# Performance work log

Measured on AMD Instinct MI355X. Metric: run time of the kernel, lower is better.

## Reference

```python
import jax, jax.numpy as jnp
import numpy as np

B, C, CI, T, H, W = 2, 1024, 512, 32, 14, 14
N = T * H * W


def setup_inputs() -> dict:
    key = jax.random.key(0)
    ks = jax.random.split(key, 6)
    s_in = 1.0 / np.sqrt(C)
    s_mid = 1.0 / np.sqrt(CI)
    return {
        "x": jax.random.normal(ks[0], (B, C, T, H, W), jnp.float32),
        "Wk": jax.random.normal(ks[1], (CI, C), jnp.float32) * s_in,
        "bk": jnp.zeros((CI,), jnp.float32),
        "Wq": jax.random.normal(ks[2], (CI, C), jnp.float32) * s_in,
        "bq": jnp.zeros((CI,), jnp.float32),
        "Wv": jax.random.normal(ks[3], (CI, C), jnp.float32) * s_in,
        "bv": jnp.zeros((CI,), jnp.float32),
        "Wo": jax.random.normal(ks[4], (C, CI), jnp.float32) * s_mid,
        "bo": jnp.zeros((C,), jnp.float32),
    }


def reference(x, Wk, bk, Wq, bq, Wv, bv, Wo, bo):
    # x: (B, C, T, H, W). Dropout layers are identity at inference.
    b, c, t, h, w = x.shape
    n = t * h * w
    xf = x.reshape(b, c, n)                          # (B, C, N)
    k = jnp.einsum("dc,bcn->bdn", Wk, xf) + bk[None, :, None]   # (B, CI, N)
    q = jnp.einsum("dc,bcn->bdn", Wq, xf) + bq[None, :, None]   # (B, CI, N)
    v = jnp.einsum("dc,bcn->bdn", Wv, xf) + bv[None, :, None]   # (B, CI, N)
    # alpha[b,i,j] = sum_d key[b,i,d] * query[b,d,j], scaled by 1/T
    alpha = jnp.einsum("bdi,bdj->bij", k, q) / float(t)          # (B, N, N)
    alpha = jax.nn.softmax(alpha, axis=-1)
    # y (B, CI, N) with y[b,c,i] = sum_j alpha[b,i,j] * v[b,c,j]
    y = jnp.einsum("bij,bcj->bci", alpha, v)
    out = jnp.einsum("dc,bcn->bdn", Wo, y) + bo[None, :, None]   # (B, C, N)
    return out.reshape(b, c, t, h, w) + x
```

## Files before the change

kernel.cpp:

```cpp
#include <hip/hip_runtime.h>

#define Bb 2
#define Cc 1024
#define CIi 512
#define Nn 6272
#define JH 3136
#define SCALE (1.0f / 32.0f)

typedef __bf16 bf16;
typedef __bf16 bf16x8 __attribute__((ext_vector_type(8)));
typedef float f32x4 __attribute__((ext_vector_type(4)));
typedef unsigned int u32;
typedef unsigned char u8;
typedef unsigned int u32x4 __attribute__((ext_vector_type(4)));

__device__ __forceinline__ void g2l16(const void* g, void* l) {
  __builtin_amdgcn_global_load_lds(
      (const __attribute__((address_space(1))) u32*)g,
      (__attribute__((address_space(3))) u32*)(size_t)l, 16, 0, 0);
}

__device__ __forceinline__ u8 to_fp8(float v) {
  return (u8)(__builtin_amdgcn_cvt_pk_fp8_f32(v, v, 0, 0) & 0xff);
}

__global__ __launch_bounds__(256) void xpose_kernel(const float* __restrict__ x,
                                                    bf16* __restrict__ xT) {
  __shared__ float tile[32][33];
  int b = blockIdx.z;
  int n0 = blockIdx.x * 32, c0 = blockIdx.y * 32;
  int tn = threadIdx.x & 31, tr = threadIdx.x >> 5;
  const float* xp = x + ((size_t)b * Cc + c0) * Nn + n0;
  for (int i = 0; i < 4; i++) {
    int c = tr + i * 8;
    tile[c][tn] = xp[(size_t)c * Nn + tn];
  }
  __syncthreads();
  bf16* op = xT + ((size_t)b * Nn + n0) * Cc + c0;
  for (int i = 0; i < 4; i++) {
    int n = tr + i * 8;
    op[(size_t)n * Cc + tn] = (bf16)tile[tn][n];
  }
}

__global__ __launch_bounds__(256) void proj_kernel(
    const bf16* __restrict__ xT, const float* __restrict__ Wk,
    const float* __restrict__ Wq, const float* __restrict__ Wv,
    const float* __restrict__ bk, const float* __restrict__ bq,
    const float* __restrict__ bv, u8* __restrict__ kT8, u8* __restrict__ qT8,
    bf16* __restrict__ vv) {
  int z = blockIdx.z;
  int b = z / 3, proj = z % 3;
  const float* W = proj == 0 ? Wk : (proj == 1 ? Wq : Wv);
  const float* bias = proj == 0 ? bk : (proj == 1 ? bq : bv);
  int m0 = blockIdx.x * 128;
  int d0 = blockIdx.y * 128;
  __shared__ __align__(16) bf16 la[128 * 40];
  __shared__ __align__(16) bf16 lb[128 * 40];
  int tid = threadIdx.x;
  int wave = tid >> 6, lane = tid & 63, quad = lane >> 4, l16 = lane & 15;
  int wm = (wave >> 1) * 64, wn = (wave & 1) * 64;
  int row2 = tid >> 1, half = tid & 1;

  f32x4 acc[4][4] = {};
  const bf16* aSrc = xT + ((size_t)b * Nn + m0) * Cc;
  const float* bSrc = W + (size_t)(d0 + row2) * Cc;

  for (int k0 = 0; k0 < Cc; k0 += 32) {
    const u32x4* ga = (const u32x4*)(aSrc + (size_t)row2 * Cc + k0 + half * 16);
    u32x4 a0 = ga[0], a1 = ga[1];
    const f32x4* gb = (const f32x4*)(bSrc + k0 + half * 16);
    f32x4 w0 = gb[0], w1 = gb[1], w2 = gb[2], w3 = gb[3];
    *(u32x4*)&la[row2 * 40 + half * 16] = a0;
    *(u32x4*)&la[row2 * 40 + half * 16 + 8] = a1;
    bf16x8 p0 = {(bf16)w0[0], (bf16)w0[1], (bf16)w0[2], (bf16)w0[3],
                 (bf16)w1[0], (bf16)w1[1], (bf16)w1[2], (bf16)w1[3]};
    bf16x8 p1 = {(bf16)w2[0], (bf16)w2[1], (bf16)w2[2], (bf16)w2[3],
                 (bf16)w3[0], (bf16)w3[1], (bf16)w3[2], (bf16)w3[3]};
    *(bf16x8*)&lb[row2 * 40 + half * 16] = p0;
    *(bf16x8*)&lb[row2 * 40 + half * 16 + 8] = p1;
    __syncthreads();
    bf16x8 af[4], bfr[4];
    for (int t = 0; t < 4; t++)
      af[t] = *(const bf16x8*)&la[(wm + t * 16 + l16) * 40 + quad * 8];
    for (int t = 0; t < 4; t++)
      bfr[t] = *(const bf16x8*)&lb[(wn + t * 16 + l16) * 40 + quad * 8];
    for (int tm = 0; tm < 4; tm++)
      for (int tn = 0; tn < 4; tn++)
        acc[tm][tn] = __builtin_amdgcn_mfma_f32_16x16x32_bf16(
            af[tm], bfr[tn], acc[tm][tn], 0, 0, 0);
    __syncthreads();
  }
  for (int tn = 0; tn < 4; tn++) {
    int dcol = d0 + wn + tn * 16 + l16;
    float bval = bias[dcol];
    for (int tm = 0; tm < 4; tm++) {
      int nbase = m0 + wm + tm * 16 + quad * 4;
      for (int r = 0; r < 4; r++) {
        float val = acc[tm][tn][r] + bval;
        int nrow = nbase + r;
        if (proj == 0) {
          kT8[((size_t)b * Nn + nrow) * CIi + dcol] = to_fp8(val);
        } else if (proj == 1) {
          int ch = (dcol >> 3) ^ (nrow & 15);
          qT8[((size_t)b * Nn + nrow) * CIi + ch * 8 + (dcol & 7)] =
              to_fp8(val);
        } else {
          vv[((size_t)b * CIi + dcol) * Nn + nrow] = (bf16)val;
        }
      }
    }
  }
}

__global__ __launch_bounds__(512, 2) void attn_kernel(
    const u8* __restrict__ kT8, const u8* __restrict__ qT8,
    const bf16* __restrict__ vv, bf16* __restrict__ yp,
    float* __restrict__ ml) {
  int l = blockIdx.x;
  int jh = l & 1, b = (l >> 1) & 1;
  int i0 = (l >> 2) * 128;
  int tid = threadIdx.x;
  int wave = tid >> 6, lane = tid & 63, quad = lane >> 4, l16 = lane & 15;
  int wi = wave & 3, wj = wave >> 2;
  int dw = wave * 64;

  __shared__ __align__(16) u8 lq[2][64 * 512];
  __shared__ __align__(16) bf16 Psm[128 * 72];
  __shared__ float redw[2][128];
  __shared__ float redi[128];

  const u8* qb = qT8 + ((size_t)b * Nn + (size_t)jh * JH) * CIi;
  const bf16* vb = vv + (size_t)b * CIi * Nn + (size_t)jh * JH;

  long kf[2][16];
  {
    const u8* kp =
        kT8 + ((size_t)b * Nn + i0 + wi * 32 + l16) * CIi + quad * 8;
#pragma unroll
    for (int h = 0; h < 2; h++)
#pragma unroll
      for (int kk = 0; kk < 16; kk++)
        kf[h][kk] = *(const long*)(kp + (size_t)(h * 16) * CIi + kk * 32);
  }
  f32x4 oacc[8][4] = {};
  f32x4 l_acc[2] = {};

  {
    const u8* qrow = qb + (size_t)(wave * 8) * CIi + lane * 16;
#pragma unroll
    for (int r = 0; r < 4; r++)
      g2l16(qrow + r * 1024, &lq[0][(wave * 8) * 512 + r * 1024]);
  }
  __syncthreads();

  for (int j0 = 0; j0 < JH; j0 += 64) {
    int t = (j0 >> 6) & 1;
    u32x4 vf0[4];
#pragma unroll
    for (int ds = 0; ds < 4; ds++)
      vf0[ds] = *(const u32x4*)(vb + (size_t)(dw + ds * 16 + l16) * Nn + j0 +
                                quad * 8);
    __builtin_amdgcn_sched_barrier(0);
    if (j0 + 64 < JH) {
      const u8* qrow = qb + (size_t)(j0 + 64 + wave * 8) * CIi + lane * 16;
#pragma unroll
      for (int r = 0; r < 4; r++)
        g2l16(qrow + r * 1024, &lq[t ^ 1][(wave * 8) * 512 + r * 1024]);
    }
    f32x4 s00 = {}, s01 = {}, s10 = {}, s11 = {};
    {
      const u8* q0 = &lq[t][(wj * 32 + l16) * 512];
      const u8* q1 = &lq[t][(wj * 32 + 16 + l16) * 512];
#pragma unroll
      for (int kk = 0; kk < 16; kk++) {
        int sl = ((kk * 4 + quad) ^ l16) * 8;
        long qf0 = *(const long*)(q0 + sl);
        long qf1 = *(const long*)(q1 + sl);
        s00 = __builtin_amdgcn_mfma_f32_16x16x32_fp8_fp8(kf[0][kk], qf0, s00,
                                                         0, 0, 0);
        s01 = __builtin_amdgcn_mfma_f32_16x16x32_fp8_fp8(kf[0][kk], qf1, s01,
                                                         0, 0, 0);
        s10 = __builtin_amdgcn_mfma_f32_16x16x32_fp8_fp8(kf[1][kk], qf0, s10,
                                                         0, 0, 0);
        s11 = __builtin_amdgcn_mfma_f32_16x16x32_fp8_fp8(kf[1][kk], qf1, s11,
                                                         0, 0, 0);
      }
    }
    {
#pragma unroll
      for (int h = 0; h < 2; h++)
#pragma unroll
        for (int jb = 0; jb < 2; jb++) {
          const f32x4& sv = h == 0 ? (jb == 0 ? s00 : s01)
                                   : (jb == 0 ? s10 : s11);
#pragma unroll
          for (int r = 0; r < 4; r++) {
            float p = __expf(fminf(fmaf(sv[r], SCALE, -2.0f), 20.0f));
            l_acc[h][r] += p;
            int gi = wi * 32 + h * 16 + quad * 4 + r;
            int gj = wj * 32 + jb * 16 + l16;
            Psm[gi * 72 + gj] = (bf16)p;
          }
        }
    }
    asm volatile("s_waitcnt lgkmcnt(0)" ::: "memory");
    __builtin_amdgcn_s_barrier();
    asm volatile("" ::: "memory");

    {
#pragma unroll
      for (int is = 0; is < 8; is++) {
        bf16x8 pf = *(const bf16x8*)&Psm[(is * 16 + l16) * 72 + quad * 8];
#pragma unroll
        for (int ds = 0; ds < 4; ds++)
          oacc[is][ds] = __builtin_amdgcn_mfma_f32_16x16x32_bf16(
              pf, __builtin_bit_cast(bf16x8, vf0[ds]), oacc[is][ds], 0, 0, 0);
      }
      u32x4 vf1[4];
#pragma unroll
      for (int ds = 0; ds < 4; ds++)
        vf1[ds] = *(const u32x4*)(vb + (size_t)(dw + ds * 16 + l16) * Nn + j0 +
                                  32 + quad * 8);
#pragma unroll
      for (int is = 0; is < 8; is++) {
        bf16x8 pf =
            *(const bf16x8*)&Psm[(is * 16 + l16) * 72 + 32 + quad * 8];
#pragma unroll
        for (int ds = 0; ds < 4; ds++)
          oacc[is][ds] = __builtin_amdgcn_mfma_f32_16x16x32_bf16(
              pf, __builtin_bit_cast(bf16x8, vf1[ds]), oacc[is][ds], 0, 0, 0);
      }
    }
    __syncthreads();
  }

#pragma unroll
  for (int o = 1; o < 16; o <<= 1)
#pragma unroll
    for (int h = 0; h < 2; h++)
#pragma unroll
      for (int r = 0; r < 4; r++) l_acc[h][r] += __shfl_xor(l_acc[h][r], o);
  if (l16 == 0) {
#pragma unroll
    for (int h = 0; h < 2; h++)
#pragma unroll
      for (int r = 0; r < 4; r++)
        redw[wj][wi * 32 + h * 16 + quad * 4 + r] = l_acc[h][r];
  }
  __syncthreads();
  if (tid < 128) {
    float s = redw[0][tid] + redw[1][tid];
    ml[(size_t)(jh * Bb + b) * Nn + i0 + tid] = s;
    redi[tid] = 1.0f / s;
  }
  __syncthreads();
  bf16* ypb = yp + ((size_t)jh * Bb + b) * Nn * CIi;
#pragma unroll
  for (int is = 0; is < 8; is++) {
    f32x4 inv = *(const f32x4*)&redi[is * 16 + quad * 4];
#pragma unroll
    for (int ds = 0; ds < 4; ds++)
#pragma unroll
      for (int r = 0; r < 4; r++)
        ypb[(size_t)(i0 + is * 16 + quad * 4 + r) * CIi + dw + ds * 16 + l16] =
            (bf16)(oacc[is][ds][r] * inv[r]);
  }
}

__global__ __launch_bounds__(256) void merge_kernel(const bf16* __restrict__ yp,
                                                    const float* __restrict__ ml,
                                                    bf16* __restrict__ y) {
  int idx = blockIdx.x * 256 + threadIdx.x;
  int row = idx >> 6, c = idx & 63;
  float l0 = ml[row];
  float l1 = ml[(size_t)Bb * Nn + row];
  float inv = 1.0f / (l0 + l1);
  float w0 = l0 * inv, w1 = l1 * inv;
  bf16x8 v0 = *(const bf16x8*)&yp[(size_t)row * CIi + c * 8];
  bf16x8 v1 =
      *(const bf16x8*)&yp[(size_t)Bb * Nn * CIi + (size_t)row * CIi + c * 8];
  bf16x8 o;
#pragma unroll
  for (int k = 0; k < 8; k++)
    o[k] = (bf16)(w0 * (float)v0[k] + w1 * (float)v1[k]);
  *(bf16x8*)&y[(size_t)row * CIi + c * 8] = o;
}

__global__ __launch_bounds__(256) void out_kernel(
    const bf16* __restrict__ y, const float* __restrict__ Wo,
    const float* __restrict__ bo, const float* __restrict__ x,
    float* __restrict__ out) {
  int b = blockIdx.z;
  int d0 = blockIdx.x * 128;
  int m0 = blockIdx.y * 128;
  __shared__ __align__(16) bf16 la[128 * 40];
  __shared__ __align__(16) bf16 lb[128 * 40];
  int tid = threadIdx.x;
  int wave = tid >> 6, lane = tid & 63, quad = lane >> 4, l16 = lane & 15;
  int wm = (wave >> 1) * 64, wn = (wave & 1) * 64;
  int row2 = tid >> 1, half = tid & 1;
  f32x4 acc[4][4] = {};
  const float* aSrc = Wo + (size_t)(d0 + row2) * CIi;
  const bf16* bSrc = y + ((size_t)b * Nn + m0 + row2) * CIi;
  for (int k0 = 0; k0 < CIi; k0 += 32) {
    const f32x4* ga = (const f32x4*)(aSrc + k0 + half * 16);
    f32x4 w0 = ga[0], w1 = ga[1], w2 = ga[2], w3 = ga[3];
    const u32x4* gb = (const u32x4*)(bSrc + k0 + half * 16);
    u32x4 b0 = gb[0], b1 = gb[1];
    bf16x8 p0 = {(bf16)w0[0], (bf16)w0[1], (bf16)w0[2], (bf16)w0[3],
                 (bf16)w1[0], (bf16)w1[1], (bf16)w1[2], (bf16)w1[3]};
    bf16x8 p1 = {(bf16)w2[0], (bf16)w2[1], (bf16)w2[2], (bf16)w2[3],
                 (bf16)w3[0], (bf16)w3[1], (bf16)w3[2], (bf16)w3[3]};
    *(bf16x8*)&la[row2 * 40 + half * 16] = p0;
    *(bf16x8*)&la[row2 * 40 + half * 16 + 8] = p1;
    *(u32x4*)&lb[row2 * 40 + half * 16] = b0;
    *(u32x4*)&lb[row2 * 40 + half * 16 + 8] = b1;
    __syncthreads();
    bf16x8 af[4], bfr[4];
    for (int t = 0; t < 4; t++)
      af[t] = *(const bf16x8*)&la[(wm + t * 16 + l16) * 40 + quad * 8];
    for (int t = 0; t < 4; t++)
      bfr[t] = *(const bf16x8*)&lb[(wn + t * 16 + l16) * 40 + quad * 8];
    for (int tm = 0; tm < 4; tm++)
      for (int tn = 0; tn < 4; tn++)
        acc[tm][tn] = __builtin_amdgcn_mfma_f32_16x16x32_bf16(
            af[tm], bfr[tn], acc[tm][tn], 0, 0, 0);
    __syncthreads();
  }
  for (int tm = 0; tm < 4; tm++) {
    for (int r = 0; r < 4; r++) {
      int drow = d0 + wm + tm * 16 + quad * 4 + r;
      float bval = bo[drow];
      const float* xrow = x + ((size_t)b * Cc + drow) * Nn;
      float* orow = out + ((size_t)b * Cc + drow) * Nn;
      for (int tn = 0; tn < 4; tn++) {
        int ncol = m0 + wn + tn * 16 + l16;
        orow[ncol] = acc[tm][tn][r] + bval + xrow[ncol];
      }
    }
  }
}

extern "C" void kernel_launch(void* const* d_in, const int* in_sizes, int n_in,
                              void* d_out, int out_size, void* d_ws,
                              size_t ws_size, hipStream_t stream) {
  (void)in_sizes;
  (void)n_in;
  (void)out_size;
  (void)ws_size;
  const float* x = (const float*)d_in[0];
  const float* Wk = (const float*)d_in[1];
  const float* bk = (const float*)d_in[2];
  const float* Wq = (const float*)d_in[3];
  const float* bq = (const float*)d_in[4];
  const float* Wv = (const float*)d_in[5];
  const float* bv = (const float*)d_in[6];
  const float* Wo = (const float*)d_in[7];
  const float* bo = (const float*)d_in[8];
  float* out = (float*)d_out;

  bf16* xT = (bf16*)d_ws;
  bf16* yp = (bf16*)d_ws;
  bf16* y = (bf16*)d_ws + (size_t)Bb * Nn * Cc;
  u8* kT8 = (u8*)d_out;
  u8* qT8 = kT8 + (size_t)Bb * Nn * CIi;
  bf16* vv = (bf16*)(qT8 + (size_t)Bb * Nn * CIi);
  float* ml = (float*)((char*)d_out + (size_t)40 * 1024 * 1024);

  xpose_kernel<<<dim3(Nn / 32, Cc / 32, Bb), 256, 0, stream>>>(x, xT);
  proj_kernel<<<dim3(Nn / 128, CIi / 128, 3 * Bb), 256, 0, stream>>>(
      xT, Wk, Wq, Wv, bk, bq, bv, kT8, qT8, vv);
  attn_kernel<<<dim3((Nn / 128) * 2 * Bb), 512, 0, stream>>>(kT8, qT8, vv, yp,
                                                             ml);
  merge_kernel<<<dim3(Bb * Nn * 64 / 256), 256, 0, stream>>>(yp, ml, y);
  out_kernel<<<dim3(Cc / 128, Nn / 128, Bb), 256, 0, stream>>>(y, Wo, bo, x,
                                                               out);
}
```

Baseline: 598.7 us.

## Give each wave full 16-row by 64-column score strip, drop cross-wave row-sum reduction

Changes the QK^T work split so each of the 8 waves owns 16 query-key rows across all 64 columns instead of a 32x32 sub-block, halving K fragment registers and removing the cross-wave redw reduction and one barrier at the end. Both V fragment halves are now loaded up front at the start of each iteration instead of loading the second half mid-PV. This trades fewer K registers for more LDS Q reads per wave (4 Q rows per kk instead of 2) and more live V registers.

```diff
diff --git a/kernel.cpp b/kernel.cpp
--- a/kernel.cpp
+++ b/kernel.cpp
@@ -122,29 +122,25 @@
   int i0 = (l >> 2) * 128;
   int tid = threadIdx.x;
   int wave = tid >> 6, lane = tid & 63, quad = lane >> 4, l16 = lane & 15;
-  int wi = wave & 3, wj = wave >> 2;
   int dw = wave * 64;
 
   __shared__ __align__(16) u8 lq[2][64 * 512];
   __shared__ __align__(16) bf16 Psm[128 * 72];
-  __shared__ float redw[2][128];
   __shared__ float redi[128];
 
   const u8* qb = qT8 + ((size_t)b * Nn + (size_t)jh * JH) * CIi;
   const bf16* vb = vv + (size_t)b * CIi * Nn + (size_t)jh * JH;
 
-  long kf[2][16];
+  long kf[16];
   {
-    const u8* kp =
-        kT8 + ((size_t)b * Nn + i0 + wi * 32 + l16) * CIi + quad * 8;
-#pragma unroll
-    for (int h = 0; h < 2; h++)
-#pragma unroll
-      for (int kk = 0; kk < 16; kk++)
-        kf[h][kk] = *(const long*)(kp + (size_t)(h * 16) * CIi + kk * 32);
+    const u8* kp = kT8 + ((size_t)b * Nn + i0 + wave * 16 + l16) * CIi +
+                   quad * 8;
+#pragma unroll
+    for (int kk = 0; kk < 16; kk++)
+      kf[kk] = *(const long*)(kp + kk * 32);
   }
   f32x4 oacc[8][4] = {};
-  f32x4 l_acc[2] = {};
+  f32x4 l_acc = {};
 
   {
     const u8* qrow = qb + (size_t)(wave * 8) * CIi + lane * 16;
@@ -156,11 +152,13 @@
 
   for (int j0 = 0; j0 < JH; j0 += 64) {
     int t = (j0 >> 6) & 1;
-    u32x4 vf0[4];
-#pragma unroll
-    for (int ds = 0; ds < 4; ds++)
-      vf0[ds] = *(const u32x4*)(vb + (size_t)(dw + ds * 16 + l16) * Nn + j0 +
-                                quad * 8);
+    u32x4 vf[2][4];
+#pragma unroll
+    for (int jc = 0; jc < 2; jc++)
+#pragma unroll
+      for (int ds = 0; ds < 4; ds++)
+        vf[jc][ds] = *(const u32x4*)(vb + (size_t)(dw + ds * 16 + l16) * Nn +
+                                     j0 + jc * 32 + quad * 8);
     __builtin_amdgcn_sched_barrier(0);
     if (j0 + 64 < JH) {
       const u8* qrow = qb + (size_t)(j0 + 64 + wave * 8) * CIi + lane * 16;
@@ -168,91 +166,68 @@
       for (int r = 0; r < 4; r++)
         g2l16(qrow + r * 1024, &lq[t ^ 1][(wave * 8) * 512 + r * 1024]);
     }
-    f32x4 s00 = {}, s01 = {}, s10 = {}, s11 = {};
+    f32x4 s[4] = {};
     {
-      const u8* q0 = &lq[t][(wj * 32 + l16) * 512];
-      const u8* q1 = &lq[t][(wj * 32 + 16 + l16) * 512];
+      const u8* q0 = &lq[t][l16 * 512];
 #pragma unroll
       for (int kk = 0; kk < 16; kk++) {
         int sl = ((kk * 4 + quad) ^ l16) * 8;
         long qf0 = *(const long*)(q0 + sl);
-        long qf1 = *(const long*)(q1 + sl);
-        s00 = __builtin_amdgcn_mfma_f32_16x16x32_fp8_fp8(kf[0][kk], qf0, s00,
-                                                         0, 0, 0);
-        s01 = __builtin_amdgcn_mfma_f32_16x16x32_fp8_fp8(kf[0][kk], qf1, s01,
-                                                         0, 0, 0);
-        s10 = __builtin_amdgcn_mfma_f32_16x16x32_fp8_fp8(kf[1][kk], qf0, s10,
-                                                         0, 0, 0);
-        s11 = __builtin_amdgcn_mfma_f32_16x16x32_fp8_fp8(kf[1][kk], qf1, s11,
-                                                         0, 0, 0);
+        long qf1 = *(const long*)(q0 + 16 * 512 + sl);
+        long qf2 = *(const long*)(q0 + 32 * 512 + sl);
+        long qf3 = *(const long*)(q0 + 48 * 512 + sl);
+        s[0] = __builtin_amdgcn_mfma_f32_16x16x32_fp8_fp8(kf[kk], qf0, s[0],
+                                                          0, 0, 0);
+        s[1] = __builtin_amdgcn_mfma_f32_16x16x32_fp8_fp8(kf[kk], qf1, s[1],
+                                                          0, 0, 0);
+        s[2] = __builtin_amdgcn_mfma_f32_16x16x32_fp8_fp8(kf[kk], qf2, s[2],
+                                                          0, 0, 0);
+        s[3] = __builtin_amdgcn_mfma_f32_16x16x32_fp8_fp8(kf[kk], qf3, s[3],
+                                                          0, 0, 0);
       }
     }
     {
 #pragma unroll
-      for (int h = 0; h < 2; h++)
-#pragma unroll
-        for (int jb = 0; jb < 2; jb++) {
-          const f32x4& sv = h == 0 ? (jb == 0 ? s00 : s01)
-                                   : (jb == 0 ? s10 : s11);
-#pragma unroll
-          for (int r = 0; r < 4; r++) {
-            float p = __expf(fminf(fmaf(sv[r], SCALE, -2.0f), 20.0f));
-            l_acc[h][r] += p;
-            int gi = wi * 32 + h * 16 + quad * 4 + r;
-            int gj = wj * 32 + jb * 16 + l16;
-            Psm[gi * 72 + gj] = (bf16)p;
-          }
+      for (int jb = 0; jb < 4; jb++)
+#pragma unroll
+        for (int r = 0; r < 4; r++) {
+          float p = __expf(fminf(fmaf(s[jb][r], SCALE, -2.0f), 20.0f));
+          l_acc[r] += p;
+          int gi = wave * 16 + quad * 4 + r;
+          int gj = jb * 16 + l16;
+          Psm[gi * 72 + gj] = (bf16)p;
         }
     }
     asm volatile("s_waitcnt lgkmcnt(0)" ::: "memory");
     __builtin_amdgcn_s_barrier();
     asm volatile("" ::: "memory");
 
-    {
+#pragma unroll
+    for (int jc = 0; jc < 2; jc++)
 #pragma unroll
       for (int is = 0; is < 8; is++) {
-        bf16x8 pf = *(const bf16x8*)&Psm[(is * 16 + l16) * 72 + quad * 8];
+        bf16x8 pf = *(const bf16x8*)&Psm[(is * 16 + l16) * 72 + jc * 32 +
+                                         quad * 8];
 #pragma unroll
         for (int ds = 0; ds < 4; ds++)
           oacc[is][ds] = __builtin_amdgcn_mfma_f32_16x16x32_bf16(
-              pf, __builtin_bit_cast(bf16x8, vf0[ds]), oacc[is][ds], 0, 0, 0);
+              pf, __builtin_bit_cast(bf16x8, vf[jc][ds]), oacc[is][ds], 0, 0,
+              0);
       }
-      u32x4 vf1[4];
-#pragma unroll
-      for (int ds = 0; ds < 4; ds++)
-        vf1[ds] = *(const u32x4*)(vb + (size_t)(dw + ds * 16 + l16) * Nn + j0 +
-                                  32 + quad * 8);
-#pragma unroll
-      for (int is = 0; is < 8; is++) {
-        bf16x8 pf =
-            *(const bf16x8*)&Psm[(is * 16 + l16) * 72 + 32 + quad * 8];
-#pragma unroll
-        for (int ds = 0; ds < 4; ds++)
-          oacc[is][ds] = __builtin_amdgcn_mfma_f32_16x16x32_bf16(
-              pf, __builtin_bit_cast(bf16x8, vf1[ds]), oacc[is][ds], 0, 0, 0);
-      }
-    }
     __syncthreads();
   }
 
 #pragma unroll
   for (int o = 1; o < 16; o <<= 1)
 #pragma unroll
-    for (int h = 0; h < 2; h++)
-#pragma unroll
-      for (int r = 0; r < 4; r++) l_acc[h][r] += __shfl_xor(l_acc[h][r], o);
+    for (int r = 0; r < 4; r++) l_acc[r] += __shfl_xor(l_acc[r], o);
   if (l16 == 0) {
 #pragma unroll
-    for (int h = 0; h < 2; h++)
-#pragma unroll
-      for (int r = 0; r < 4; r++)
-        redw[wj][wi * 32 + h * 16 + quad * 4 + r] = l_acc[h][r];
-  }
-  __syncthreads();
-  if (tid < 128) {
-    float s = redw[0][tid] + redw[1][tid];
-    ml[(size_t)(jh * Bb + b) * Nn + i0 + tid] = s;
-    redi[tid] = 1.0f / s;
+    for (int r = 0; r < 4; r++) {
+      int gi = wave * 16 + quad * 4 + r;
+      ml[(size_t)(jh * Bb + b) * Nn + i0 + gi] = l_acc[r];
+      redi[gi] = 1.0f / l_acc[r];
+    }
   }
   __syncthreads();
   bf16* ypb = yp + ((size_t)jh * Bb + b) * Nn * CIi;
```

Result: faster. 520.0 us (-13.1%).
